# Kernel optimization log

Hardware: AMD Instinct MI355X
Metric: run time of the kernel (lower is better)

## Reference

```python
import jax, jax.numpy as jnp
import numpy as np

INPUT_SIZE = 1024
HIDDEN_SIZE = 1024
BATCH = 32768
LEARNING_RATE = 0.01
# First call: time_stamps is empty -> temporal_weight = 1.0
TEMPORAL_WEIGHT = 1.0


def setup_inputs() -> dict:
    key = jax.random.key(0)
    kx, kw = jax.random.split(key)
    x = jax.random.normal(kx, (BATCH, INPUT_SIZE), dtype=jnp.float32)
    # nn.Parameter(torch.randn(input_size, hidden_size) * 0.1)
    W = jax.random.normal(kw, (INPUT_SIZE, HIDDEN_SIZE), dtype=jnp.float32) * 0.1
    return {"x": x, "W": W}


def reference(x, W):
    # Forward: hidden = tanh(x @ W)
    hidden = jnp.tanh(x @ W)  # [B, H]
    # Hebbian update: sum_b lr * outer(x_b, hidden_b) * w(t) / B == lr * w(t)/B * x^T @ hidden
    batch = x.shape[0]
    delta_w = (LEARNING_RATE * TEMPORAL_WEIGHT / batch) * (x.T @ hidden)  # [I, H]
    new_W = jnp.clip(W + delta_w, -1.0, 1.0)
    return hidden, new_W
```

## Files before the change

### kernel.cpp

```cpp
#include <hip/hip_runtime.h>
#include <cstdint>

#define BB 32768
#define II 1024
#define HH 1024
#define SPLIT 16
#define KCH (BB/SPLIT)
#define NT1 (II/64)
#define NT2 (KCH/64)

typedef _Float16 f16;
typedef _Float16 f16x4 __attribute__((ext_vector_type(4)));
typedef _Float16 f16x8 __attribute__((ext_vector_type(8)));
typedef float f32x4 __attribute__((ext_vector_type(4)));

typedef const __attribute__((address_space(1))) void gvoid_t;
typedef __attribute__((address_space(3))) void lvoid_t;

__device__ __forceinline__ void gload16(const void* g, void* l){
    __builtin_amdgcn_global_load_lds((gvoid_t*)g, (lvoid_t*)l, 16, 0, 0);
}

__device__ __forceinline__ float tanh_fast(float s){
    float a = fabsf(s);
    float e = __expf(-2.0f * a);
    float t = __fdividef(1.0f - e, 1.0f + e);
    return s < 0.0f ? -t : t;
}

__global__ __launch_bounds__(256) void k_prep2(const float* __restrict__ x,
                                               f16* __restrict__ xf,
                                               f16* __restrict__ xt,
                                               const float* __restrict__ W,
                                               f16* __restrict__ wt){
    __shared__ float lt[64*67];
    const int t = threadIdx.x;
    const int bx = (int)blockIdx.x;
    const float* in; f16* cvt; f16* tr; int C, R, r0;
    if (bx < 512){ in = x; cvt = xf; tr = xt; C = II; R = BB; r0 = bx*64; }
    else         { in = W; cvt = nullptr; tr = wt; C = HH; R = II; r0 = (bx-512)*64; }
    const int c0 = blockIdx.y*64;
    #pragma unroll
    for (int p=0; p<4; ++p){
        int r = p*16 + (t>>4);
        int c = (t&15)*4;
        f32x4 v = __builtin_nontemporal_load((const f32x4*)&in[(size_t)(r0+r)*C + c0 + c]);
        if (cvt){
            f16x4 hv = {(f16)v[0],(f16)v[1],(f16)v[2],(f16)v[3]};
            *(f16x4*)&cvt[(size_t)(r0+r)*C + c0 + c] = hv;
        }
        lt[r*67 + c+0] = v[0];
        lt[r*67 + c+1] = v[1];
        lt[r*67 + c+2] = v[2];
        lt[r*67 + c+3] = v[3];
    }
    __syncthreads();
    const int c = t>>2, rb = (t&3)*16;
    f16x8 a, b;
    #pragma unroll
    for (int e=0; e<8; ++e) a[e] = (f16)lt[(rb+e)*67 + c];
    #pragma unroll
    for (int e=0; e<8; ++e) b[e] = (f16)lt[(rb+8+e)*67 + c];
    f16* o = &tr[(size_t)(c0+c)*R + r0 + rb];
    *(f16x8*)o = a;
    *(f16x8*)(o+8) = b;
}

template<bool MT>
__device__ __forceinline__ void stage_half(const f16* __restrict__ panel, int ld,
                                           int row0, int kcol0, char* lds_half,
                                           int wid, int lane){
    #pragma unroll
    for (int r=0;r<2;++r){
        int o = r*8192 + wid*1024 + lane*16;
        int rr = o>>7;
        int c0 = (o&127) ^ ((rr&7)<<4);
        if constexpr (!MT){
            const f16* src = panel + (size_t)(row0 + rr)*ld + kcol0 + (c0>>1);
            gload16(src, lds_half + r*8192 + wid*1024);
        } else {
            int h    = row0 + rr;
            int babs = kcol0 + (c0>>1);
            const f16* src = panel + (((size_t)(h>>4)*(BB>>4) + (babs>>4))<<8)
                                   + ((h&15)<<4) + (babs&8);
            gload16(src, lds_half + r*8192 + wid*1024);
        }
    }
}

#define RD_A(BUFA, mh) { \
    _Pragma("unroll") for (int m_=0;m_<4;++m_){ \
        af[m_][0] = *(const f16x8*)((BUFA) + rowA + (mh)*8192 + m_*2048 + ksw0); \
        af[m_][1] = *(const f16x8*)((BUFA) + rowA + (mh)*8192 + m_*2048 + ksw1); }}

#define RD_B(BUFB, nh) { \
    _Pragma("unroll") for (int n_=0;n_<2;++n_){ \
        bf[(nh)*2+n_][0] = *(const f16x8*)((BUFB) + rowB + (nh)*4096 + n_*2048 + ksw0); \
        bf[(nh)*2+n_][1] = *(const f16x8*)((BUFB) + rowB + (nh)*4096 + n_*2048 + ksw1); }}

#define MFMA_Q(mh,nh) { \
    __builtin_amdgcn_s_setprio(1); \
    _Pragma("unroll") for (int m_=0;m_<4;++m_){ \
      _Pragma("unroll") for (int n_=0;n_<2;++n_){ \
        _Pragma("unroll") for (int ks_=0;ks_<2;++ks_){ \
          acc[(mh)*4+m_][(nh)*2+n_] = __builtin_amdgcn_mfma_f32_16x16x32_f16( \
              af[m_][ks_], bf[(nh)*2+n_][ks_], acc[(mh)*4+m_][(nh)*2+n_], 0,0,0); }}} \
    __builtin_amdgcn_s_setprio(0); }

#define PH_SYNC1 { __builtin_amdgcn_s_barrier(); \
    asm volatile("s_waitcnt lgkmcnt(0)" ::: "memory"); \
    __builtin_amdgcn_sched_barrier(0); }
#define PH_SYNC2 { __builtin_amdgcn_s_barrier(); }
#define LGKM8 { asm volatile("s_waitcnt lgkmcnt(8)" ::: "memory"); }

template<bool BMT>
__device__ __forceinline__ void kloop8(const f16* __restrict__ Ap, int lda, int arow0,
                                       const f16* __restrict__ Bp, int ldb, int brow0,
                                       int kbase, int nt, char* sm,
                                       f32x4 (&acc)[8][4])
{
    const int t = threadIdx.x, lane = t & 63, wid = t >> 6;
    const int wr = wid >> 2, wc = wid & 3;
    const int fr = lane & 15, kg = lane >> 4;
    const int mask = nt - 1;
    char* const A0 = sm;
    char* const B0 = sm + 32768;
    char* const A1 = sm + 65536;
    char* const B1 = sm + 98304;
    const int rowA = wr*16384 + fr*128;
    const int rowB = (wc>>1)*16384 + (wc&1)*8192 + fr*128;
    const int ksw0 = ((kg    ) ^ (fr & 7)) << 4;
    const int ksw1 = ((kg + 4) ^ (fr & 7)) << 4;

    f16x8 af[4][2], bf[4][2];

    stage_half<false>(Ap, lda, arow0 +   0, kbase +  0, A0,         wid, lane);
    stage_half<false>(Ap, lda, arow0 + 128, kbase +  0, A0 + 16384, wid, lane);
    stage_half<BMT  >(Bp, ldb, brow0 +   0, kbase +  0, B0,         wid, lane);
    stage_half<BMT  >(Bp, ldb, brow0 + 128, kbase +  0, B0 + 16384, wid, lane);
    stage_half<BMT  >(Bp, ldb, brow0 +   0, kbase + 64, B1,         wid, lane);
    stage_half<false>(Ap, lda, arow0 +   0, kbase + 64, A1,         wid, lane);
    asm volatile("s_waitcnt vmcnt(4)" ::: "memory");
    __builtin_amdgcn_s_barrier();

    const int ni = nt >> 1;
    for (int it = 0; it < ni; ++it){
        const int k1 = (2*it + 1) * 64;
        const int k2 = ((2*it + 2) & mask) * 64;
        const int k3 = ((2*it + 3) & mask) * 64;
        RD_A(A0, 0); RD_B(B0, 0);
        stage_half<false>(Ap, lda, arow0 + 128, kbase + k1, A1 + 16384, wid, lane);
        LGKM8; PH_SYNC1; MFMA_Q(0,0); PH_SYNC2;
        RD_B(B0, 1);
        stage_half<BMT>(Bp, ldb, brow0 + 128, kbase + k1, B1 + 16384, wid, lane);
        PH_SYNC1; MFMA_Q(0,1); PH_SYNC2;
        RD_A(A0, 1);
        stage_half<BMT>(Bp, ldb, brow0 +   0, kbase + k2, B0, wid, lane);
        PH_SYNC1; MFMA_Q(1,0); PH_SYNC2;
        stage_half<false>(Ap, lda, arow0 +   0, kbase + k2, A0, wid, lane);
        PH_SYNC1; MFMA_Q(1,1);
        asm volatile("s_waitcnt vmcnt(4)" ::: "memory");
        __builtin_amdgcn_s_barrier();
        RD_A(A1, 0); RD_B(B1, 0);
        stage_half<false>(Ap, lda, arow0 + 128, kbase + k2, A0 + 16384, wid, lane);
        LGKM8; PH_SYNC1; MFMA_Q(0,0); PH_SYNC2;
        RD_B(B1, 1);
        stage_half<BMT>(Bp, ldb, brow0 + 128, kbase + k2, B0 + 16384, wid, lane);
        PH_SYNC1; MFMA_Q(0,1); PH_SYNC2;
        RD_A(A1, 1);
        stage_half<BMT>(Bp, ldb, brow0 +   0, kbase + k3, B1, wid, lane);
        PH_SYNC1; MFMA_Q(1,0); PH_SYNC2;
        stage_half<false>(Ap, lda, arow0 +   0, kbase + k3, A1, wid, lane);
        PH_SYNC1; MFMA_Q(1,1);
        asm volatile("s_waitcnt vmcnt(4)" ::: "memory");
        __builtin_amdgcn_s_barrier();
    }
    asm volatile("s_waitcnt vmcnt(0)" ::: "memory");
    __builtin_amdgcn_s_barrier();
}

__global__ __launch_bounds__(512,2) void k_gemm1(const f16* __restrict__ xf,
                                                 const f16* __restrict__ wt,
                                                 float* __restrict__ hidden,
                                                 f16* __restrict__ ht){
    __shared__ char sm[131072];
    const int bid = (int)blockIdx.x;
    const int swz = (bid & 7)*64 + (bid >> 3);
    const int btile = swz >> 2, htile = swz & 3;
    f32x4 acc[8][4] = {};
    kloop8<false>(xf, II, btile*256, wt, II, htile*256, 0, NT1, sm, acc);

    const int t = threadIdx.x, lane = t & 63, wid = t >> 6;
    const int wr = wid >> 2, wc = wid & 3;
    const int fr = lane & 15, kg = lane >> 4;
    const int b_base = btile*256 + wr*128 + kg*4;
    const int h_base = htile*256 + wc*64 + fr;
    #pragma unroll
    for (int mf=0; mf<8; ++mf){
        const int b = b_base + mf*16;
        #pragma unroll
        for (int nf=0; nf<4; ++nf){
            const int h = h_base + nf*16;
            float t0 = tanh_fast(acc[mf][nf][0]);
            float t1 = tanh_fast(acc[mf][nf][1]);
            float t2 = tanh_fast(acc[mf][nf][2]);
            float t3 = tanh_fast(acc[mf][nf][3]);
            f16x4 hv = {(f16)t0,(f16)t1,(f16)t2,(f16)t3};
            *(f16x4*)&ht[(((size_t)(h>>4)*(BB>>4) + (b>>4))<<8) + ((h&15)<<4) + (b&15)] = hv;
            hidden[(size_t)(b+0)*HH + h] = t0;
            hidden[(size_t)(b+1)*HH + h] = t1;
            hidden[(size_t)(b+2)*HH + h] = t2;
            hidden[(size_t)(b+3)*HH + h] = t3;
        }
    }
}

__global__ __launch_bounds__(512,2) void k_gemm2(const f16* __restrict__ xt,
                                                 const f16* __restrict__ ht,
                                                 f16* __restrict__ part){
    __shared__ char sm[131072];
    const int bid = (int)blockIdx.x;
    const int swz = (bid & 7)*32 + (bid >> 3);
    const int split = swz >> 4, tile = swz & 15;
    const int itile = tile & 3, htile = tile >> 2;
    f32x4 acc[8][4] = {};
    kloop8<true>(xt, BB, itile*256, ht, BB, htile*256, split*KCH, NT2, sm, acc);

    const int t = threadIdx.x, lane = t & 63, wid = t >> 6;
    const int wr = wid >> 2, wc = wid & 3;
    const int fr = lane & 15, kg = lane >> 4;
    const size_t pb = (size_t)split*II*HH;
    #pragma unroll
    for (int mf=0; mf<8; ++mf){
        const int i0 = itile*256 + wr*128 + mf*16 + kg*4;
        #pragma unroll
        for (int nf=0; nf<4; ++nf){
            const int h = htile*256 + wc*64 + nf*16 + fr;
            f16x4 pv = {(f16)acc[mf][nf][0],(f16)acc[mf][nf][1],
                        (f16)acc[mf][nf][2],(f16)acc[mf][nf][3]};
            *(f16x4*)&part[pb + (((size_t)(i0>>4)*(HH>>4) + (h>>4))<<8) + ((h&15)<<4) + (i0&15)] = pv;
        }
    }
}

__global__ __launch_bounds__(256) void k_final(const f16* __restrict__ part,
                                               const float* __restrict__ W,
                                               float* __restrict__ outW){
    const int T = (int)blockIdx.x*256 + threadIdx.x;
    const int mt = T >> 5;
    const int hl = (T & 31) >> 1;
    const int ihalf = T & 1;
    const int i0 = (mt >> 6)*16 + ihalf*8;
    const int h  = (mt & 63)*16 + hl;
    const size_t po = ((size_t)mt << 8) + (hl << 4) + ihalf*8;
    float s[8] = {};
    #pragma unroll
    for (int sp=0; sp<SPLIT; ++sp){
        f16x8 p = __builtin_nontemporal_load((const f16x8*)&part[(size_t)sp*1048576 + po]);
        #pragma unroll
        for (int e=0;e<8;++e) s[e] += (float)p[e];
    }
    const float SCALE = 3.0517578125e-07f;
    #pragma unroll
    for (int e=0;e<8;++e){
        const size_t o = (size_t)(i0+e)*HH + h;
        float r = fminf(1.f, fmaxf(-1.f, fmaf(SCALE, s[e], W[o])));
        __builtin_nontemporal_store(r, &outW[o]);
    }
}

extern "C" void kernel_launch(void* const* d_in, const int* in_sizes, int n_in,
                              void* d_out, int out_size, void* d_ws, size_t ws_size,
                              hipStream_t stream){
    (void)in_sizes; (void)n_in; (void)out_size; (void)ws_size;
    const float* x = (const float*)d_in[0];
    const float* W = (const float*)d_in[1];
    float* hidden = (float*)d_out;
    float* outW   = hidden + (size_t)BB*HH;
    char* ws = (char*)d_ws;
    f16* xf   = (f16*)(ws);
    f16* xt   = (f16*)(ws + 67108864ull);
    f16* ht   = (f16*)(ws + 134217728ull);
    f16* wt   = (f16*)(ws + 201326592ull);
    f16* part = (f16*)(ws);

    k_prep2<<<dim3(528, 16), 256, 0, stream>>>(x, xf, xt, W, wt);
    k_gemm1<<<dim3((BB/256)*(HH/256)), 512, 0, stream>>>(xf, wt, hidden, ht);
    k_gemm2<<<dim3(16*SPLIT), 512, 0, stream>>>(xt, ht, part);
    k_final<<<dim3((II*HH)/(256*8)), 256, 0, stream>>>(part, W, outW);
}
```

Measured before the change: 207.0 us.

## Rewrite gemm1 with 256x128 tiles, K=32 double buffering and higher occupancy

```diff
diff --git a/kernel.cpp b/kernel.cpp
--- a/kernel.cpp
+++ b/kernel.cpp
@@ -6,7 +6,7 @@
 #define HH 1024
 #define SPLIT 16
 #define KCH (BB/SPLIT)
-#define NT1 (II/64)
+#define NT1_32 (II/32)
 #define NT2 (KCH/64)
 
 typedef _Float16 f16;
@@ -64,6 +64,104 @@
     f16* o = &tr[(size_t)(c0+c)*R + r0 + rb];
     *(f16x8*)o = a;
     *(f16x8*)(o+8) = b;
+}
+
+__device__ __forceinline__ void stageA32(const f16* __restrict__ panel, int ld,
+                                         int row0, int kcol, char* buf,
+                                         int wid, int lane){
+    #pragma unroll
+    for (int s=0; s<2; ++s){
+        int o  = s*8192 + wid*1024 + lane*16;
+        int rr = o>>6;
+        int c  = (o&63) ^ ((rr&3)<<4);
+        gload16(panel + (size_t)(row0+rr)*ld + kcol + (c>>1), buf + s*8192 + wid*1024);
+    }
+}
+__device__ __forceinline__ void stageB32(const f16* __restrict__ panel, int ld,
+                                         int row0, int kcol, char* buf,
+                                         int wid, int lane){
+    int o  = wid*1024 + lane*16;
+    int rr = o>>6;
+    int c  = (o&63) ^ ((rr&3)<<4);
+    gload16(panel + (size_t)(row0+rr)*ld + kcol + (c>>1), buf + wid*1024);
+}
+
+__global__ __launch_bounds__(512,4) void k_gemm1(const f16* __restrict__ xf,
+                                                 const f16* __restrict__ wt,
+                                                 float* __restrict__ hidden,
+                                                 f16* __restrict__ ht){
+    __shared__ char sm[49152];
+    char* const A0 = sm;
+    char* const A1 = sm + 16384;
+    char* const B0 = sm + 32768;
+    char* const B1 = sm + 40960;
+    const int bid = (int)blockIdx.x;
+    const int swz = (bid & 7)*128 + (bid >> 3);
+    const int btile = swz >> 3, htile = swz & 7;
+    const int arow0 = btile*256, brow0 = htile*128;
+
+    const int t = threadIdx.x, lane = t & 63, wid = t >> 6;
+    const int wr = wid >> 2, wc = wid & 3;
+    const int fr = lane & 15, kg = lane >> 4;
+    const int rowA = (wr*128 + fr)*64;
+    const int rowB = (wc*32 + fr)*64;
+    const int ksw  = ((kg ^ (fr & 3)) << 4);
+
+    f32x4 acc[8][2] = {};
+    f16x8 af[8], bf[2];
+
+    stageA32(xf, II, arow0, 0, A0, wid, lane);
+    stageB32(wt, II, brow0, 0, B0, wid, lane);
+    asm volatile("s_waitcnt vmcnt(0)" ::: "memory");
+    __builtin_amdgcn_s_barrier();
+
+    for (int tt = 0; tt < NT1_32; ++tt){
+        char* const Ac = (tt & 1) ? A1 : A0;
+        char* const Bc = (tt & 1) ? B1 : B0;
+        char* const An = (tt & 1) ? A0 : A1;
+        char* const Bn = (tt & 1) ? B0 : B1;
+        #pragma unroll
+        for (int m=0;m<8;++m) af[m] = *(const f16x8*)(Ac + rowA + m*1024 + ksw);
+        #pragma unroll
+        for (int n=0;n<2;++n) bf[n] = *(const f16x8*)(Bc + rowB + n*1024 + ksw);
+        if (tt + 1 < NT1_32){
+            stageA32(xf, II, arow0, (tt+1)*32, An, wid, lane);
+            stageB32(wt, II, brow0, (tt+1)*32, Bn, wid, lane);
+        }
+        __builtin_amdgcn_s_barrier();
+        asm volatile("s_waitcnt lgkmcnt(0)" ::: "memory");
+        __builtin_amdgcn_sched_barrier(0);
+        __builtin_amdgcn_s_setprio(1);
+        #pragma unroll
+        for (int m=0;m<8;++m)
+            #pragma unroll
+            for (int n=0;n<2;++n)
+                acc[m][n] = __builtin_amdgcn_mfma_f32_16x16x32_f16(af[m], bf[n], acc[m][n], 0, 0, 0);
+        __builtin_amdgcn_s_setprio(0);
+        asm volatile("s_waitcnt vmcnt(0)" ::: "memory");
+        __builtin_amdgcn_s_barrier();
+    }
+
+    const int b_base = btile*256 + wr*128 + kg*4;
+    const int h_base = htile*128 + wc*32 + fr;
+    #pragma unroll
+    for (int mf=0; mf<8; ++mf){
+        const int b = b_base + mf*16;
+        #pragma unroll
+        for (int nf=0; nf<2; ++nf){
+            const int h = h_base + nf*16;
+            float t0 = tanh_fast(acc[mf][nf][0]);
+            float t1 = tanh_fast(acc[mf][nf][1]);
+            float t2 = tanh_fast(acc[mf][nf][2]);
+            float t3 = tanh_fast(acc[mf][nf][3]);
+            f16x4 hv = {(f16)t0,(f16)t1,(f16)t2,(f16)t3};
+            *(f16x4*)&ht[(((size_t)(h>>4)*(BB>>4) + (b>>4))<<8) + ((h&15)<<4) + (b&15)] = hv;
+            hidden[(size_t)(b+0)*HH + h] = t0;
+            hidden[(size_t)(b+1)*HH + h] = t1;
+            hidden[(size_t)(b+2)*HH + h] = t2;
+            hidden[(size_t)(b+3)*HH + h] = t3;
+        }
+    }
 }
 
 template<bool MT>
@@ -179,42 +277,6 @@
     __builtin_amdgcn_s_barrier();
 }
 
-__global__ __launch_bounds__(512,2) void k_gemm1(const f16* __restrict__ xf,
-                                                 const f16* __restrict__ wt,
-                                                 float* __restrict__ hidden,
-                                                 f16* __restrict__ ht){
-    __shared__ char sm[131072];
-    const int bid = (int)blockIdx.x;
-    const int swz = (bid & 7)*64 + (bid >> 3);
-    const int btile = swz >> 2, htile = swz & 3;
-    f32x4 acc[8][4] = {};
-    kloop8<false>(xf, II, btile*256, wt, II, htile*256, 0, NT1, sm, acc);
-
-    const int t = threadIdx.x, lane = t & 63, wid = t >> 6;
-    const int wr = wid >> 2, wc = wid & 3;
-    const int fr = lane & 15, kg = lane >> 4;
-    const int b_base = btile*256 + wr*128 + kg*4;
-    const int h_base = htile*256 + wc*64 + fr;
-    #pragma unroll
-    for (int mf=0; mf<8; ++mf){
-        const int b = b_base + mf*16;
-        #pragma unroll
-        for (int nf=0; nf<4; ++nf){
-            const int h = h_base + nf*16;
-            float t0 = tanh_fast(acc[mf][nf][0]);
-            float t1 = tanh_fast(acc[mf][nf][1]);
-            float t2 = tanh_fast(acc[mf][nf][2]);
-            float t3 = tanh_fast(acc[mf][nf][3]);
-            f16x4 hv = {(f16)t0,(f16)t1,(f16)t2,(f16)t3};
-            *(f16x4*)&ht[(((size_t)(h>>4)*(BB>>4) + (b>>4))<<8) + ((h&15)<<4) + (b&15)] = hv;
-            hidden[(size_t)(b+0)*HH + h] = t0;
-            hidden[(size_t)(b+1)*HH + h] = t1;
-            hidden[(size_t)(b+2)*HH + h] = t2;
-            hidden[(size_t)(b+3)*HH + h] = t3;
-        }
-    }
-}
-
 __global__ __launch_bounds__(512,2) void k_gemm2(const f16* __restrict__ xt,
                                                  const f16* __restrict__ ht,
                                                  f16* __restrict__ part){
@@ -285,7 +347,7 @@
     f16* part = (f16*)(ws);
 
     k_prep2<<<dim3(528, 16), 256, 0, stream>>>(x, xf, xt, W, wt);
-    k_gemm1<<<dim3((BB/256)*(HH/256)), 512, 0, stream>>>(xf, wt, hidden, ht);
+    k_gemm1<<<dim3((BB/256)*(HH/128)), 512, 0, stream>>>(xf, wt, hidden, ht);
     k_gemm2<<<dim3(16*SPLIT), 512, 0, stream>>>(xt, ht, part);
     k_final<<<dim3((II*HH)/(256*8)), 256, 0, stream>>>(part, W, outW);
 }
```

Result: slower. 225.5 us (+8.9%).

## Run Hebbian x^T·hidden GEMM in FP8 with fp8 transposed operands

Applied to the files above, without the earlier changes.

```diff
diff --git a/kernel.cpp b/kernel.cpp
--- a/kernel.cpp
+++ b/kernel.cpp
@@ -1,4 +1,5 @@
 #include <hip/hip_runtime.h>
+#include <hip/hip_fp8.h>
 #include <cstdint>
 
 #define BB 32768
@@ -28,26 +29,32 @@
     return s < 0.0f ? -t : t;
 }
 
+__device__ __forceinline__ unsigned char f2fp8(float v){
+    __hip_fp8_e4m3 q(v);
+    return (unsigned char)q.__x;
+}
+
 __global__ __launch_bounds__(256) void k_prep2(const float* __restrict__ x,
                                                f16* __restrict__ xf,
-                                               f16* __restrict__ xt,
+                                               unsigned char* __restrict__ xt8,
                                                const float* __restrict__ W,
                                                f16* __restrict__ wt){
     __shared__ float lt[64*67];
     const int t = threadIdx.x;
     const int bx = (int)blockIdx.x;
-    const float* in; f16* cvt; f16* tr; int C, R, r0;
-    if (bx < 512){ in = x; cvt = xf; tr = xt; C = II; R = BB; r0 = bx*64; }
-    else         { in = W; cvt = nullptr; tr = wt; C = HH; R = II; r0 = (bx-512)*64; }
+    const bool isX = (bx < 512);
+    const float* in = isX ? x : W;
+    const int C = isX ? II : HH, R = isX ? BB : II;
+    const int r0 = (isX ? bx : bx-512)*64;
     const int c0 = blockIdx.y*64;
     #pragma unroll
     for (int p=0; p<4; ++p){
         int r = p*16 + (t>>4);
         int c = (t&15)*4;
         f32x4 v = __builtin_nontemporal_load((const f32x4*)&in[(size_t)(r0+r)*C + c0 + c]);
-        if (cvt){
+        if (isX){
             f16x4 hv = {(f16)v[0],(f16)v[1],(f16)v[2],(f16)v[3]};
-            *(f16x4*)&cvt[(size_t)(r0+r)*C + c0 + c] = hv;
+            *(f16x4*)&xf[(size_t)(r0+r)*C + c0 + c] = hv;
         }
         lt[r*67 + c+0] = v[0];
         lt[r*67 + c+1] = v[1];
@@ -56,17 +63,23 @@
     }
     __syncthreads();
     const int c = t>>2, rb = (t&3)*16;
-    f16x8 a, b;
-    #pragma unroll
-    for (int e=0; e<8; ++e) a[e] = (f16)lt[(rb+e)*67 + c];
-    #pragma unroll
-    for (int e=0; e<8; ++e) b[e] = (f16)lt[(rb+8+e)*67 + c];
-    f16* o = &tr[(size_t)(c0+c)*R + r0 + rb];
-    *(f16x8*)o = a;
-    *(f16x8*)(o+8) = b;
-}
-
-template<bool MT>
+    if (isX){
+        union { unsigned char cb[16]; f32x4 v4; } u;
+        #pragma unroll
+        for (int e=0; e<16; ++e) u.cb[e] = f2fp8(lt[(rb+e)*67 + c]);
+        *(f32x4*)&xt8[(size_t)(c0+c)*R + r0 + rb] = u.v4;
+    } else {
+        f16x8 a, b;
+        #pragma unroll
+        for (int e=0; e<8; ++e) a[e] = (f16)lt[(rb+e)*67 + c];
+        #pragma unroll
+        for (int e=0; e<8; ++e) b[e] = (f16)lt[(rb+8+e)*67 + c];
+        f16* o = &wt[(size_t)(c0+c)*R + r0 + rb];
+        *(f16x8*)o = a;
+        *(f16x8*)(o+8) = b;
+    }
+}
+
 __device__ __forceinline__ void stage_half(const f16* __restrict__ panel, int ld,
                                            int row0, int kcol0, char* lds_half,
                                            int wid, int lane){
@@ -75,16 +88,7 @@
         int o = r*8192 + wid*1024 + lane*16;
         int rr = o>>7;
         int c0 = (o&127) ^ ((rr&7)<<4);
-        if constexpr (!MT){
-            const f16* src = panel + (size_t)(row0 + rr)*ld + kcol0 + (c0>>1);
-            gload16(src, lds_half + r*8192 + wid*1024);
-        } else {
-            int h    = row0 + rr;
-            int babs = kcol0 + (c0>>1);
-            const f16* src = panel + (((size_t)(h>>4)*(BB>>4) + (babs>>4))<<8)
-                                   + ((h&15)<<4) + (babs&8);
-            gload16(src, lds_half + r*8192 + wid*1024);
-        }
+        gload16(panel + (size_t)(row0 + rr)*ld + kcol0 + (c0>>1), lds_half + r*8192 + wid*1024);
     }
 }
 
@@ -113,11 +117,10 @@
 #define PH_SYNC2 { __builtin_amdgcn_s_barrier(); }
 #define LGKM8 { asm volatile("s_waitcnt lgkmcnt(8)" ::: "memory"); }
 
-template<bool BMT>
-__device__ __forceinline__ void kloop8(const f16* __restrict__ Ap, int lda, int arow0,
-                                       const f16* __restrict__ Bp, int ldb, int brow0,
-                                       int kbase, int nt, char* sm,
-                                       f32x4 (&acc)[8][4])
+__device__ __forceinline__ void kloop8_f16(const f16* __restrict__ Ap, int lda, int arow0,
+                                           const f16* __restrict__ Bp, int ldb, int brow0,
+                                           int kbase, int nt, char* sm,
+                                           f32x4 (&acc)[8][4])
 {
     const int t = threadIdx.x, lane = t & 63, wid = t >> 6;
     const int wr = wid >> 2, wc = wid & 3;
@@ -134,12 +137,12 @@
 
     f16x8 af[4][2], bf[4][2];
 
-    stage_half<false>(Ap, lda, arow0 +   0, kbase +  0, A0,         wid, lane);
-    stage_half<false>(Ap, lda, arow0 + 128, kbase +  0, A0 + 16384, wid, lane);
-    stage_half<BMT  >(Bp, ldb, brow0 +   0, kbase +  0, B0,         wid, lane);
-    stage_half<BMT  >(Bp, ldb, brow0 + 128, kbase +  0, B0 + 16384, wid, lane);
-    stage_half<BMT  >(Bp, ldb, brow0 +   0, kbase + 64, B1,         wid, lane);
-    stage_half<false>(Ap, lda, arow0 +   0, kbase + 64, A1,         wid, lane);
+    stage_half(Ap, lda, arow0 +   0, kbase +  0, A0,         wid, lane);
+    stage_half(Ap, lda, arow0 + 128, kbase +  0, A0 + 16384, wid, lane);
+    stage_half(Bp, ldb, brow0 +   0, kbase +  0, B0,         wid, lane);
+    stage_half(Bp, ldb, brow0 + 128, kbase +  0, B0 + 16384, wid, lane);
+    stage_half(Bp, ldb, brow0 +   0, kbase + 64, B1,         wid, lane);
+    stage_half(Ap, lda, arow0 +   0, kbase + 64, A1,         wid, lane);
     asm volatile("s_waitcnt vmcnt(4)" ::: "memory");
     __builtin_amdgcn_s_barrier();
 
@@ -149,28 +152,28 @@
         const int k2 = ((2*it + 2) & mask) * 64;
         const int k3 = ((2*it + 3) & mask) * 64;
         RD_A(A0, 0); RD_B(B0, 0);
-        stage_half<false>(Ap, lda, arow0 + 128, kbase + k1, A1 + 16384, wid, lane);
+        stage_half(Ap, lda, arow0 + 128, kbase + k1, A1 + 16384, wid, lane);
         LGKM8; PH_SYNC1; MFMA_Q(0,0); PH_SYNC2;
         RD_B(B0, 1);
-        stage_half<BMT>(Bp, ldb, brow0 + 128, kbase + k1, B1 + 16384, wid, lane);
+        stage_half(Bp, ldb, brow0 + 128, kbase + k1, B1 + 16384, wid, lane);
         PH_SYNC1; MFMA_Q(0,1); PH_SYNC2;
         RD_A(A0, 1);
-        stage_half<BMT>(Bp, ldb, brow0 +   0, kbase + k2, B0, wid, lane);
+        stage_half(Bp, ldb, brow0 +   0, kbase + k2, B0, wid, lane);
         PH_SYNC1; MFMA_Q(1,0); PH_SYNC2;
-        stage_half<false>(Ap, lda, arow0 +   0, kbase + k2, A0, wid, lane);
+        stage_half(Ap, lda, arow0 +   0, kbase + k2, A0, wid, lane);
         PH_SYNC1; MFMA_Q(1,1);
         asm volatile("s_waitcnt vmcnt(4)" ::: "memory");
         __builtin_amdgcn_s_barrier();
         RD_A(A1, 0); RD_B(B1, 0);
-        stage_half<false>(Ap, lda, arow0 + 128, kbase + k2, A0 + 16384, wid, lane);
+        stage_half(Ap, lda, arow0 + 128, kbase + k2, A0 + 16384, wid, lane);
         LGKM8; PH_SYNC1; MFMA_Q(0,0); PH_SYNC2;
         RD_B(B1, 1);
-        stage_half<BMT>(Bp, ldb, brow0 + 128, kbase + k2, B0 + 16384, wid, lane);
+        stage_half(Bp, ldb, brow0 + 128, kbase + k2, B0 + 16384, wid, lane);
         PH_SYNC1; MFMA_Q(0,1); PH_SYNC2;
         RD_A(A1, 1);
-        stage_half<BMT>(Bp, ldb, brow0 +   0, kbase + k3, B1, wid, lane);
+        stage_half(Bp, ldb, brow0 +   0, kbase + k3, B1, wid, lane);
         PH_SYNC1; MFMA_Q(1,0); PH_SYNC2;
-        stage_half<false>(Ap, lda, arow0 +   0, kbase + k3, A1, wid, lane);
+        stage_half(Ap, lda, arow0 +   0, kbase + k3, A1, wid, lane);
         PH_SYNC1; MFMA_Q(1,1);
         asm volatile("s_waitcnt vmcnt(4)" ::: "memory");
         __builtin_amdgcn_s_barrier();
@@ -182,13 +185,13 @@
 __global__ __launch_bounds__(512,2) void k_gemm1(const f16* __restrict__ xf,
                                                  const f16* __restrict__ wt,
                                                  float* __restrict__ hidden,
-                                                 f16* __restrict__ ht){
+                                                 unsigned char* __restrict__ ht8){
     __shared__ char sm[131072];
     const int bid = (int)blockIdx.x;
     const int swz = (bid & 7)*64 + (bid >> 3);
     const int btile = swz >> 2, htile = swz & 3;
     f32x4 acc[8][4] = {};
-    kloop8<false>(xf, II, btile*256, wt, II, htile*256, 0, NT1, sm, acc);
+    kloop8_f16(xf, II, btile*256, wt, II, htile*256, 0, NT1, sm, acc);
 
     const int t = threadIdx.x, lane = t & 63, wid = t >> 6;
     const int wr = wid >> 2, wc = wid & 3;
@@ -205,8 +208,10 @@
             float t1 = tanh_fast(acc[mf][nf][1]);
             float t2 = tanh_fast(acc[mf][nf][2]);
             float t3 = tanh_fast(acc[mf][nf][3]);
-            f16x4 hv = {(f16)t0,(f16)t1,(f16)t2,(f16)t3};
-            *(f16x4*)&ht[(((size_t)(h>>4)*(BB>>4) + (b>>4))<<8) + ((h&15)<<4) + (b&15)] = hv;
+            union { unsigned char cb[4]; unsigned int u; } p;
+            p.cb[0] = f2fp8(t0); p.cb[1] = f2fp8(t1);
+            p.cb[2] = f2fp8(t2); p.cb[3] = f2fp8(t3);
+            *(unsigned int*)&ht8[(((size_t)(h>>4)*(BB>>4) + (b>>4))<<8) + ((h&15)<<4) + (b&15)] = p.u;
             hidden[(size_t)(b+0)*HH + h] = t0;
             hidden[(size_t)(b+1)*HH + h] = t1;
             hidden[(size_t)(b+2)*HH + h] = t2;
@@ -215,20 +220,113 @@
     }
 }
 
-__global__ __launch_bounds__(512,2) void k_gemm2(const f16* __restrict__ xt,
-                                                 const f16* __restrict__ ht,
+template<bool MT>
+__device__ __forceinline__ void stage_half8(const unsigned char* __restrict__ panel, int ld,
+                                            int row0, int kcol0, char* lds_half,
+                                            int wid, int lane){
+    int o  = wid*1024 + lane*16;
+    int rr = o>>6;
+    int c  = (o&63) ^ ((rr&6)<<3);
+    if constexpr (!MT){
+        gload16(panel + (size_t)(row0+rr)*ld + kcol0 + c, lds_half + wid*1024);
+    } else {
+        int h = row0 + rr;
+        int babs = kcol0 + c;
+        gload16(panel + (((size_t)(h>>4)*(BB>>4) + (babs>>4))<<8) + ((h&15)<<4) + (babs&15),
+                lds_half + wid*1024);
+    }
+}
+
+#define RD_A8(BUFA, mh) { \
+    _Pragma("unroll") for (int m_=0;m_<4;++m_){ \
+        afl[m_][0] = *(const long*)((BUFA) + rowA8 + (mh)*4096 + m_*1024 + k80); \
+        afl[m_][1] = *(const long*)((BUFA) + rowA8 + (mh)*4096 + m_*1024 + k81); }}
+
+#define RD_B8(BUFB, nh) { \
+    _Pragma("unroll") for (int n_=0;n_<2;++n_){ \
+        bfl[(nh)*2+n_][0] = *(const long*)((BUFB) + rowB8 + (nh)*2048 + n_*1024 + k80); \
+        bfl[(nh)*2+n_][1] = *(const long*)((BUFB) + rowB8 + (nh)*2048 + n_*1024 + k81); }}
+
+#define MFMA_Q8(mh,nh) { \
+    __builtin_amdgcn_s_setprio(1); \
+    _Pragma("unroll") for (int m_=0;m_<4;++m_){ \
+      _Pragma("unroll") for (int n_=0;n_<2;++n_){ \
+        _Pragma("unroll") for (int ks_=0;ks_<2;++ks_){ \
+          acc[(mh)*4+m_][(nh)*2+n_] = __builtin_amdgcn_mfma_f32_16x16x32_fp8_fp8( \
+              afl[m_][ks_], bfl[(nh)*2+n_][ks_], acc[(mh)*4+m_][(nh)*2+n_], 0,0,0); }}} \
+    __builtin_amdgcn_s_setprio(0); }
+
+__global__ __launch_bounds__(512,2) void k_gemm2(const unsigned char* __restrict__ xt8,
+                                                 const unsigned char* __restrict__ ht8,
                                                  f16* __restrict__ part){
-    __shared__ char sm[131072];
+    __shared__ char sm[65536];
     const int bid = (int)blockIdx.x;
     const int swz = (bid & 7)*32 + (bid >> 3);
     const int split = swz >> 4, tile = swz & 15;
     const int itile = tile & 3, htile = tile >> 2;
-    f32x4 acc[8][4] = {};
-    kloop8<true>(xt, BB, itile*256, ht, BB, htile*256, split*KCH, NT2, sm, acc);
+    const int arow0 = itile*256, brow0 = htile*256, kbase = split*KCH;
 
     const int t = threadIdx.x, lane = t & 63, wid = t >> 6;
     const int wr = wid >> 2, wc = wid & 3;
     const int fr = lane & 15, kg = lane >> 4;
+    const int mask = NT2 - 1;
+    char* const A0 = sm;
+    char* const B0 = sm + 16384;
+    char* const A1 = sm + 32768;
+    char* const B1 = sm + 49152;
+    const int rowA8 = wr*8192 + fr*64;
+    const int rowB8 = (wc>>1)*8192 + (wc&1)*4096 + fr*64;
+    const int s6  = fr & 6;
+    const int k80 = ((kg    ) ^ s6) << 3;
+    const int k81 = ((kg + 4) ^ s6) << 3;
+
+    f32x4 acc[8][4] = {};
+    long afl[4][2], bfl[4][2];
+
+    stage_half8<false>(xt8, BB, arow0 +   0, kbase +  0, A0,        wid, lane);
+    stage_half8<false>(xt8, BB, arow0 + 128, kbase +  0, A0 + 8192, wid, lane);
+    stage_half8<true >(ht8, BB, brow0 +   0, kbase +  0, B0,        wid, lane);
+    stage_half8<true >(ht8, BB, brow0 + 128, kbase +  0, B0 + 8192, wid, lane);
+    stage_half8<true >(ht8, BB, brow0 +   0, kbase + 64, B1,        wid, lane);
+    stage_half8<false>(xt8, BB, arow0 +   0, kbase + 64, A1,        wid, lane);
+    asm volatile("s_waitcnt vmcnt(2)" ::: "memory");
+    __builtin_amdgcn_s_barrier();
+
+    const int ni = NT2 >> 1;
+    for (int it = 0; it < ni; ++it){
+        const int k1 = (2*it + 1) * 64;
+        const int k2 = ((2*it + 2) & mask) * 64;
+        const int k3 = ((2*it + 3) & mask) * 64;
+        RD_A8(A0, 0); RD_B8(B0, 0);
+        stage_half8<false>(xt8, BB, arow0 + 128, kbase + k1, A1 + 8192, wid, lane);
+        PH_SYNC1; MFMA_Q8(0,0); PH_SYNC2;
+        RD_B8(B0, 1);
+        stage_half8<true>(ht8, BB, brow0 + 128, kbase + k1, B1 + 8192, wid, lane);
+        PH_SYNC1; MFMA_Q8(0,1); PH_SYNC2;
+        RD_A8(A0, 1);
+        stage_half8<true>(ht8, BB, brow0 +   0, kbase + k2, B0, wid, lane);
+        PH_SYNC1; MFMA_Q8(1,0); PH_SYNC2;
+        stage_half8<false>(xt8, BB, arow0 +   0, kbase + k2, A0, wid, lane);
+        PH_SYNC1; MFMA_Q8(1,1);
+        asm volatile("s_waitcnt vmcnt(2)" ::: "memory");
+        __builtin_amdgcn_s_barrier();
+        RD_A8(A1, 0); RD_B8(B1, 0);
+        stage_half8<false>(xt8, BB, arow0 + 128, kbase + k2, A0 + 8192, wid, lane);
+        PH_SYNC1; MFMA_Q8(0,0); PH_SYNC2;
+        RD_B8(B1, 1);
+        stage_half8<true>(ht8, BB, brow0 + 128, kbase + k2, B0 + 8192, wid, lane);
+        PH_SYNC1; MFMA_Q8(0,1); PH_SYNC2;
+        RD_A8(A1, 1);
+        stage_half8<true>(ht8, BB, brow0 +   0, kbase + k3, B1, wid, lane);
+        PH_SYNC1; MFMA_Q8(1,0); PH_SYNC2;
+        stage_half8<false>(xt8, BB, arow0 +   0, kbase + k3, A1, wid, lane);
+        PH_SYNC1; MFMA_Q8(1,1);
+        asm volatile("s_waitcnt vmcnt(2)" ::: "memory");
+        __builtin_amdgcn_s_barrier();
+    }
+    asm volatile("s_waitcnt vmcnt(0)" ::: "memory");
+    __builtin_amdgcn_s_barrier();
+
     const size_t pb = (size_t)split*II*HH;
     #pragma unroll
     for (int mf=0; mf<8; ++mf){
@@ -278,14 +376,14 @@
     float* hidden = (float*)d_out;
     float* outW   = hidden + (size_t)BB*HH;
     char* ws = (char*)d_ws;
-    f16* xf   = (f16*)(ws);
-    f16* xt   = (f16*)(ws + 67108864ull);
-    f16* ht   = (f16*)(ws + 134217728ull);
-    f16* wt   = (f16*)(ws + 201326592ull);
-    f16* part = (f16*)(ws);
-
-    k_prep2<<<dim3(528, 16), 256, 0, stream>>>(x, xf, xt, W, wt);
-    k_gemm1<<<dim3((BB/256)*(HH/256)), 512, 0, stream>>>(xf, wt, hidden, ht);
-    k_gemm2<<<dim3(16*SPLIT), 512, 0, stream>>>(xt, ht, part);
+    f16*           xf   = (f16*)(ws);
+    unsigned char* xt8  = (unsigned char*)(ws + 67108864ull);
+    unsigned char* ht8  = (unsigned char*)(ws + 100663296ull);
+    f16*           wt   = (f16*)(ws + 134217728ull);
+    f16*           part = (f16*)(ws);
+
+    k_prep2<<<dim3(528, 16), 256, 0, stream>>>(x, xf, xt8, W, wt);
+    k_gemm1<<<dim3((BB/256)*(HH/256)), 512, 0, stream>>>(xf, wt, hidden, ht8);
+    k_gemm2<<<dim3(16*SPLIT), 512, 0, stream>>>(xt8, ht8, part);
     k_final<<<dim3((II*HH)/(256*8)), 256, 0, stream>>>(part, W, outW);
 }
```

Result: faster. 195.2 us (-5.7%).
